# Kernel tuning notes

Hardware: AMD Instinct MI355X
Metric: run time of the kernel (lower is better)

Reference implementation:

```python
import jax, jax.numpy as jnp
import numpy as np

SEQ, D_IN, D_OUT = 8192, 1024, 1024

def setup_inputs() -> dict:
    key = jax.random.key(0)
    kx, kq, kk, kv = jax.random.split(key, 4)
    scale = 1.0 / np.sqrt(D_IN)
    return {
        "x": jax.random.normal(kx, (SEQ, D_IN), dtype=jnp.float32),
        "Wq": jax.random.normal(kq, (D_OUT, D_IN), dtype=jnp.float32) * scale,
        "Wk": jax.random.normal(kk, (D_OUT, D_IN), dtype=jnp.float32) * scale,
        "Wv": jax.random.normal(kv, (D_OUT, D_IN), dtype=jnp.float32) * scale,
    }

def reference(x, Wq, Wk, Wv):
    # nn.Linear: y = x @ W.T (no bias)
    q = x @ Wq.T            # [S, d_out]
    k = x @ Wk.T            # [S, d_out]
    v = x @ Wv.T            # [S, d_out]
    d_k = k.shape[-1]
    scores = (q @ k.T) / jnp.sqrt(jnp.float32(d_k))   # [S, S]
    attn = jax.nn.softmax(scores, axis=-1)
    return attn @ v         # [S, d_out]
```

## Files before the change

kernel.cpp:

```cpp
#include <hip/hip_runtime.h>

typedef unsigned short ushort_t;
typedef __attribute__((ext_vector_type(8))) __bf16 bf16x8;
typedef __attribute__((ext_vector_type(4))) float f32x4;

#define SEQ 8192
#define DIN 1024
#define DOUT 1024

#define OM_BF16 0
#define OM_EXP  2
#define OM_NORM 3

__device__ __forceinline__ ushort_t f2bf(float f) {
  union { float f; unsigned u; } c; c.f = f;
  unsigned u = c.u;
  return (ushort_t)((u + 0x7fffu + ((u >> 16) & 1u)) >> 16);
}

__device__ __forceinline__ void async16(ushort_t* lds, const ushort_t* g) {
  __builtin_amdgcn_global_load_lds(
      (__attribute__((address_space(1))) void*)g,
      (__attribute__((address_space(3))) void*)lds, 16, 0, 0);
}

template <int N>
__device__ __forceinline__ void waitv() {
  asm volatile("s_waitcnt vmcnt(%0)" :: "n"(N) : "memory");
}

__global__ __launch_bounds__(256) void cvt_all_kernel(
    const float* __restrict__ x, const float* __restrict__ wq,
    const float* __restrict__ wk, const float* __restrict__ wv,
    ushort_t* __restrict__ xb, ushort_t* __restrict__ wqkb,
    ushort_t* __restrict__ wvb) {
  int b = blockIdx.x;
  const float* src;
  ushort_t* dst;
  int idx;
  if (b < 8192) {
    src = x; dst = xb; idx = b * 256 + threadIdx.x;
  } else {
    int r = b - 8192;
    int w = r >> 10;
    idx = (r & 1023) * 256 + threadIdx.x;
    if (w == 0)      { src = wq; dst = wqkb; }
    else if (w == 1) { src = wk; dst = wqkb + DOUT * DIN; }
    else             { src = wv; dst = wvb; }
  }
  float4 f = ((const float4*)src)[idx];
  ushort4 o;
  o.x = f2bf(f.x); o.y = f2bf(f.y); o.z = f2bf(f.z); o.w = f2bf(f.w);
  ((ushort4*)dst)[idx] = o;
}

__global__ __launch_bounds__(256) void rowsum_inv_kernel(const float* __restrict__ rsp,
                                                         float* __restrict__ invrs) {
  int r = blockIdx.x * 256 + threadIdx.x;
  float s = 0.f;
  #pragma unroll
  for (int p2 = 0; p2 < 32; ++p2) s += rsp[p2 * SEQ + r];
  invrs[r] = 1.0f / s;
}

template <int OUTMODE, int SUPER, int BM, int BN>
__global__ __launch_bounds__(512, 2) void gemm8p(
    const ushort_t* __restrict__ A, const ushort_t* __restrict__ B,
    void* __restrict__ C, int lda, int ldb, int ldc, int K, float scale,
    float* __restrict__ rsp, const float* __restrict__ invrs) {
  constexpr int WM = BM / 2, WN = BN / 4;
  constexpr int MI = BM / 32, NIfr = BN / 64;
  constexpr int MH = MI / 2;
  constexpr int AST = BM * 64, BST = BN * 64;
  constexpr int AHALF = AST / 2, BHALF = BST / 2;
  constexpr int LA = BM / 128, LB = BN / 128;
  __shared__ ushort_t As[2 * AST];
  __shared__ ushort_t Bs[2 * BST];

  const int t = threadIdx.x;
  const int lane = t & 63;
  const int wave = t >> 6;
  const int wr = wave >> 2, wc = wave & 3;
  const int quad = lane >> 4, r16 = lane & 15;

  const int gx = gridDim.x;
  const int nwg = gx * gridDim.y;
  const int bid = blockIdx.y * gx + blockIdx.x;
  int mt, nt;
  if (SUPER == 1) {
    int x = bid & 7, l = bid >> 3;
    mt = ((x >> 2) << 4) + ((l >> 5) << 2) + ((l >> 3) & 3);
    nt = ((x & 3) << 3) + (l & 7);
  } else {
    const int q8 = nwg >> 3;
    const int b2 = (bid & 7) * q8 + (bid >> 3);
    mt = b2 / gx;
    nt = b2 - mt * gx;
  }
  const int rowBase = mt * BM;
  const int colBase = nt * BN;

  unsigned offA[2][LA], offB[2][LB];
  #pragma unroll
  for (int h = 0; h < 2; ++h) {
    #pragma unroll
    for (int i = 0; i < LA; ++i) {
      int c = t + i * 512, row = c >> 3, sl = c & 7;
      offA[h][i] = (unsigned)((rowBase + h * (BM / 2) + row) * lda +
                              ((sl ^ (row & 7)) << 3));
    }
    #pragma unroll
    for (int i = 0; i < LB; ++i) {
      int c = t + i * 512, row = c >> 3, sl = c & 7;
      offB[h][i] = (unsigned)((colBase + h * (BN / 2) + row) * ldb +
                              ((sl ^ (row & 7)) << 3));
    }
  }

  auto stageA = [&](int buf, int h) {
    #pragma unroll
    for (int i = 0; i < LA; ++i) {
      async16(&As[buf * AST + h * AHALF + (t + i * 512) * 8], A + offA[h][i]);
      offA[h][i] += 64;
    }
  };
  auto stageB = [&](int buf, int h) {
    #pragma unroll
    for (int i = 0; i < LB; ++i) {
      async16(&Bs[buf * BST + h * BHALF + (t + i * 512) * 8], B + offB[h][i]);
      offB[h][i] += 64;
    }
  };

  f32x4 acc[MI][NIfr] = {};
  bf16x8 af[MH], b0[NIfr], b1[NIfr];

  auto readA = [&](const ushort_t* as, int mh, int ks) {
    #pragma unroll
    for (int mi = 0; mi < MH; ++mi) {
      int row = wr * WM + (mh * MH + mi) * 16 + r16;
      int sl = (ks * 4 + quad) ^ (row & 7);
      af[mi] = *(const bf16x8*)&as[(row * 8 + sl) * 8];
    }
  };
  auto readB = [&](const ushort_t* bs, int ks, bf16x8* bfr) {
    #pragma unroll
    for (int ni = 0; ni < NIfr; ++ni) {
      int row = wc * WN + ni * 16 + r16;
      int sl = (ks * 4 + quad) ^ (row & 7);
      bfr[ni] = *(const bf16x8*)&bs[(row * 8 + sl) * 8];
    }
  };
  auto presync = [&]() {
    __builtin_amdgcn_sched_barrier(0);
    __builtin_amdgcn_s_barrier();
    asm volatile("s_waitcnt lgkmcnt(0)" ::: "memory");
    __builtin_amdgcn_sched_barrier(0);
  };
  auto mfmaC = [&](int mh, const bf16x8* bfr) {
    __builtin_amdgcn_s_setprio(1);
    #pragma unroll
    for (int mi = 0; mi < MH; ++mi)
      #pragma unroll
      for (int ni = 0; ni < NIfr; ++ni)
        acc[mh * MH + mi][ni] = __builtin_amdgcn_mfma_f32_16x16x32_bf16(
            af[mi], bfr[ni], acc[mh * MH + mi][ni], 0, 0, 0);
    __builtin_amdgcn_s_setprio(0);
    __builtin_amdgcn_sched_barrier(0);
  };

  stageB(0, 0); stageB(0, 1); stageA(0, 0); stageA(0, 1);
  stageB(1, 0); stageB(1, 1);
  waitv<2 * LB>();
  __builtin_amdgcn_s_barrier();

  const int NITER = K / 128;
  for (int it = 0; it < NITER; ++it) {
    const bool more = (it + 1 < NITER);
    {
      const ushort_t* as = As;
      const ushort_t* bs = Bs;
      readA(as, 0, 0); readB(bs, 0, b0);
      stageA(1, 0);
      presync(); mfmaC(0, b0);
      __builtin_amdgcn_s_barrier();
      readB(bs, 1, b1); readA(as, 1, 0);
      stageA(1, 1);
      presync(); mfmaC(1, b0);
      __builtin_amdgcn_s_barrier();
      readA(as, 0, 1);
      if (more) stageB(0, 0);
      presync(); mfmaC(0, b1);
      __builtin_amdgcn_s_barrier();
      readA(as, 1, 1);
      if (more) stageB(0, 1);
      presync(); mfmaC(1, b1);
      if (more) waitv<2 * LB>(); else waitv<0>();
      __builtin_amdgcn_s_barrier();
    }
    {
      const ushort_t* as = As + AST;
      const ushort_t* bs = Bs + BST;
      readA(as, 0, 0); readB(bs, 0, b0);
      if (more) stageA(0, 0);
      presync(); mfmaC(0, b0);
      __builtin_amdgcn_s_barrier();
      readB(bs, 1, b1); readA(as, 1, 0);
      if (more) stageA(0, 1);
      presync(); mfmaC(1, b0);
      __builtin_amdgcn_s_barrier();
      readA(as, 0, 1);
      if (more) stageB(1, 0);
      presync(); mfmaC(0, b1);
      __builtin_amdgcn_s_barrier();
      readA(as, 1, 1);
      if (more) stageB(1, 1);
      presync(); mfmaC(1, b1);
      if (more) waitv<2 * LB>();
      __builtin_amdgcn_s_barrier();
    }
  }

  float iv[MI][4];
  if constexpr (OUTMODE == OM_NORM) {
    #pragma unroll
    for (int mi = 0; mi < MI; ++mi)
      #pragma unroll
      for (int r = 0; r < 4; ++r)
        iv[mi][r] = invrs[rowBase + wr * WM + mi * 16 + quad * 4 + r];
  }

  float psum[MI][4];
  if constexpr (OUTMODE == OM_EXP) {
    #pragma unroll
    for (int mi = 0; mi < MI; ++mi)
      #pragma unroll
      for (int r = 0; r < 4; ++r) psum[mi][r] = 0.f;
  }

  #pragma unroll
  for (int mi = 0; mi < MI; ++mi)
    #pragma unroll
    for (int ni = 0; ni < NIfr; ++ni)
      #pragma unroll
      for (int r = 0; r < 4; ++r) {
        int grow = rowBase + wr * WM + mi * 16 + quad * 4 + r;
        int gcol = colBase + wc * WN + ni * 16 + r16;
        float a = acc[mi][ni][r];
        if constexpr (OUTMODE == OM_BF16) {
          ((ushort_t*)C)[(size_t)grow * ldc + gcol] = f2bf(a * scale);
        } else if constexpr (OUTMODE == OM_EXP) {
          float e = exp2f(a * scale);
          psum[mi][r] += e;
          ((ushort_t*)C)[(size_t)grow * ldc + gcol] = f2bf(e);
        } else {
          ((float*)C)[(size_t)grow * ldc + gcol] = a * iv[mi][r];
        }
      }

  if constexpr (OUTMODE == OM_EXP) {
    __syncthreads();
    float* lds_rs = (float*)As;
    #pragma unroll
    for (int mi = 0; mi < MI; ++mi)
      #pragma unroll
      for (int r = 0; r < 4; ++r) {
        float sv = psum[mi][r];
        sv += __shfl_xor(sv, 1, 64);
        sv += __shfl_xor(sv, 2, 64);
        sv += __shfl_xor(sv, 4, 64);
        sv += __shfl_xor(sv, 8, 64);
        if (r16 == 0)
          lds_rs[wc * 256 + wr * WM + mi * 16 + quad * 4 + r] = sv;
      }
    __syncthreads();
    if (t < 256)
      rsp[(size_t)nt * SEQ + rowBase + t] =
          lds_rs[t] + lds_rs[256 + t] + lds_rs[512 + t] + lds_rs[768 + t];
  }
}

extern "C" void kernel_launch(void* const* d_in, const int* in_sizes, int n_in,
                              void* d_out, int out_size, void* d_ws, size_t ws_size,
                              hipStream_t stream) {
  const float* x  = (const float*)d_in[0];
  const float* Wq = (const float*)d_in[1];
  const float* Wk = (const float*)d_in[2];
  const float* Wv = (const float*)d_in[3];
  float* out = (float*)d_out;

  char* p = (char*)d_ws;
  ushort_t* xb   = (ushort_t*)p; p += (size_t)SEQ * DIN * 2;
  ushort_t* wqkb = (ushort_t*)p; p += (size_t)2 * DOUT * DIN * 2;
  ushort_t* wvb  = (ushort_t*)p; p += (size_t)DOUT * DIN * 2;
  ushort_t* qkb  = (ushort_t*)p; p += (size_t)SEQ * 2 * DOUT * 2;
  ushort_t* vtb  = (ushort_t*)p; p += (size_t)DOUT * SEQ * 2;
  float*    rsp  = (float*)p;    p += (size_t)64 * SEQ * 4;
  float*    irs  = (float*)p;    p += (size_t)SEQ * 4;
  ushort_t* Sb   = (ushort_t*)p; p += (size_t)SEQ * SEQ * 2;

  cvt_all_kernel<<<8192 + 3 * 1024, 256, 0, stream>>>(x, Wq, Wk, Wv, xb, wqkb, wvb);

  dim3 blk(512);
  gemm8p<OM_BF16, 0, 256, 256><<<dim3(2048 / 256, SEQ / 256), blk, 0, stream>>>(
      xb, wqkb, qkb, DIN, DIN, 2 * DOUT, DIN, 1.0f, nullptr, nullptr);

  gemm8p<OM_BF16, 0, 128, 256><<<dim3(SEQ / 256, DOUT / 128), blk, 0, stream>>>(
      wvb, xb, vtb, DIN, DIN, SEQ, DIN, 1.0f, nullptr, nullptr);

  gemm8p<OM_EXP, 1, 256, 256><<<dim3(SEQ / 256, SEQ / 256), blk, 0, stream>>>(
      qkb, qkb + DOUT, Sb, 2 * DOUT, 2 * DOUT, SEQ, DIN,
      0.03125f * 1.44269504f, rsp, nullptr);

  rowsum_inv_kernel<<<SEQ / 256, 256, 0, stream>>>(rsp, irs);

  gemm8p<OM_NORM, 0, 256, 128><<<dim3(DOUT / 128, SEQ / 256), blk, 0, stream>>>(
      Sb, vtb, out, SEQ, SEQ, DOUT, SEQ, 1.0f, nullptr, irs);
}
```

Before: 474.8 us.

## Double-buffer A register fragments and drop per-phase barrier/waitcnt syncs in GEMM loop

Splits the A fragment registers into two sets (aCur/aNxt) so the next half's LDS reads are issued before the current MFMA block runs. It also removes the presync helper (extra s_barrier, lgkmcnt(0) wait and sched_barriers) before each MFMA phase, leaving the compiler to insert waits. The aim is to overlap LDS reads with matrix instructions and cut barrier stalls. In exchange it uses more VGPRs, which may lower occupancy, and it relies on compiler-inserted waits being correct and well placed.

```diff
diff --git a/kernel.cpp b/kernel.cpp
--- a/kernel.cpp
+++ b/kernel.cpp
@@ -133,46 +133,40 @@
   };
 
   f32x4 acc[MI][NIfr] = {};
-  bf16x8 af[MH], b0[NIfr], b1[NIfr];
-
-  auto readA = [&](const ushort_t* as, int mh, int ks) {
+  bf16x8 aCur[MH], aNxt[MH], b0[NIfr], b1[NIfr];
+
+  auto readA = [&](const ushort_t* as, int mh, int ks, bf16x8* dst) {
     #pragma unroll
     for (int mi = 0; mi < MH; ++mi) {
       int row = wr * WM + (mh * MH + mi) * 16 + r16;
       int sl = (ks * 4 + quad) ^ (row & 7);
-      af[mi] = *(const bf16x8*)&as[(row * 8 + sl) * 8];
-    }
-  };
-  auto readB = [&](const ushort_t* bs, int ks, bf16x8* bfr) {
+      dst[mi] = *(const bf16x8*)&as[(row * 8 + sl) * 8];
+    }
+  };
+  auto readB = [&](const ushort_t* bs, int ks, bf16x8* dst) {
     #pragma unroll
     for (int ni = 0; ni < NIfr; ++ni) {
       int row = wc * WN + ni * 16 + r16;
       int sl = (ks * 4 + quad) ^ (row & 7);
-      bfr[ni] = *(const bf16x8*)&bs[(row * 8 + sl) * 8];
-    }
-  };
-  auto presync = [&]() {
-    __builtin_amdgcn_sched_barrier(0);
-    __builtin_amdgcn_s_barrier();
-    asm volatile("s_waitcnt lgkmcnt(0)" ::: "memory");
-    __builtin_amdgcn_sched_barrier(0);
-  };
-  auto mfmaC = [&](int mh, const bf16x8* bfr) {
+      dst[ni] = *(const bf16x8*)&bs[(row * 8 + sl) * 8];
+    }
+  };
+  auto mfmaC = [&](int mh, const bf16x8* aset, const bf16x8* bfr) {
     __builtin_amdgcn_s_setprio(1);
     #pragma unroll
     for (int mi = 0; mi < MH; ++mi)
       #pragma unroll
       for (int ni = 0; ni < NIfr; ++ni)
         acc[mh * MH + mi][ni] = __builtin_amdgcn_mfma_f32_16x16x32_bf16(
-            af[mi], bfr[ni], acc[mh * MH + mi][ni], 0, 0, 0);
+            aset[mi], bfr[ni], acc[mh * MH + mi][ni], 0, 0, 0);
     __builtin_amdgcn_s_setprio(0);
-    __builtin_amdgcn_sched_barrier(0);
   };
 
   stageB(0, 0); stageB(0, 1); stageA(0, 0); stageA(0, 1);
   stageB(1, 0); stageB(1, 1);
   waitv<2 * LB>();
   __builtin_amdgcn_s_barrier();
+  asm volatile("" ::: "memory");
 
   const int NITER = K / 128;
   for (int it = 0; it < NITER; ++it) {
@@ -180,44 +174,46 @@
     {
       const ushort_t* as = As;
       const ushort_t* bs = Bs;
-      readA(as, 0, 0); readB(bs, 0, b0);
+      readA(as, 0, 0, aCur); readB(bs, 0, b0);
+      readA(as, 1, 0, aNxt);
       stageA(1, 0);
-      presync(); mfmaC(0, b0);
-      __builtin_amdgcn_s_barrier();
-      readB(bs, 1, b1); readA(as, 1, 0);
+      mfmaC(0, aCur, b0);
+      __builtin_amdgcn_s_barrier();
+      readA(as, 0, 1, aCur); readB(bs, 1, b1);
       stageA(1, 1);
-      presync(); mfmaC(1, b0);
-      __builtin_amdgcn_s_barrier();
-      readA(as, 0, 1);
+      mfmaC(1, aNxt, b0);
+      __builtin_amdgcn_s_barrier();
+      readA(as, 1, 1, aNxt);
       if (more) stageB(0, 0);
-      presync(); mfmaC(0, b1);
-      __builtin_amdgcn_s_barrier();
-      readA(as, 1, 1);
+      mfmaC(0, aCur, b1);
+      __builtin_amdgcn_s_barrier();
       if (more) stageB(0, 1);
-      presync(); mfmaC(1, b1);
+      mfmaC(1, aNxt, b1);
       if (more) waitv<2 * LB>(); else waitv<0>();
       __builtin_amdgcn_s_barrier();
+      asm volatile("" ::: "memory");
     }
     {
       const ushort_t* as = As + AST;
       const ushort_t* bs = Bs + BST;
-      readA(as, 0, 0); readB(bs, 0, b0);
+      readA(as, 0, 0, aCur); readB(bs, 0, b0);
+      readA(as, 1, 0, aNxt);
       if (more) stageA(0, 0);
-      presync(); mfmaC(0, b0);
-      __builtin_amdgcn_s_barrier();
-      readB(bs, 1, b1); readA(as, 1, 0);
+      mfmaC(0, aCur, b0);
+      __builtin_amdgcn_s_barrier();
+      readA(as, 0, 1, aCur); readB(bs, 1, b1);
       if (more) stageA(0, 1);
-      presync(); mfmaC(1, b0);
-      __builtin_amdgcn_s_barrier();
-      readA(as, 0, 1);
+      mfmaC(1, aNxt, b0);
+      __builtin_amdgcn_s_barrier();
+      readA(as, 1, 1, aNxt);
       if (more) stageB(1, 0);
-      presync(); mfmaC(0, b1);
-      __builtin_amdgcn_s_barrier();
-      readA(as, 1, 1);
+      mfmaC(0, aCur, b1);
+      __builtin_amdgcn_s_barrier();
       if (more) stageB(1, 1);
-      presync(); mfmaC(1, b1);
+      mfmaC(1, aNxt, b1);
       if (more) waitv<2 * LB>();
       __builtin_amdgcn_s_barrier();
+      asm volatile("" ::: "memory");
     }
   }
 
```

After: 456.6 us. 3.8% less time.
